# Kernel tuning notes

Measured on AMD Instinct MI355X. Metric: run time of the kernel, lower is better.

Reference implementation:

```python
import jax, jax.numpy as jnp
import numpy as np

GAMMA = 0.5
BATCH, DIM, UNITS = 16384, 512, 1024


def setup_inputs() -> dict:
    key = jax.random.key(0)
    k1, k2 = jax.random.split(key)
    inputs = jax.random.normal(k1, (BATCH, DIM), dtype=jnp.float32)
    mu = jax.random.normal(k2, (DIM, UNITS), dtype=jnp.float32)
    return {"inputs": inputs, "mu": mu}


def reference(inputs, mu):
    # Squared L2 distance from each input row to each center (column of mu):
    x_sq = jnp.sum(inputs * inputs, axis=1, keepdims=True)        # [B, 1]
    mu_sq = jnp.sum(mu * mu, axis=0, keepdims=True)               # [1, U]
    cross = inputs @ mu                                           # [B, U] GEMM
    l2 = x_sq - 2.0 * cross + mu_sq                                # [B, U]
    return jnp.exp(-GAMMA * l2)
```

## Files before the change

kernel.cpp:

```cpp
#include <hip/hip_runtime.h>
#include <hip/hip_bf16.h>

#define BATCH 16384
#define DIM   512
#define UNITS 1024

typedef float v16f __attribute__((ext_vector_type(16)));

#define APITCH 516
#define BPITCH 33

__device__ __forceinline__ void async_copy16(const void* g, void* l) {
    __builtin_amdgcn_global_load_lds(
        (const __attribute__((address_space(1))) void*)g,
        (__attribute__((address_space(3))) void*)l,
        16 , 0 , 0 );
}

__global__ __launch_bounds__(256)
void prep_kernel(const float* __restrict__ in, const float* __restrict__ mu,
                 unsigned char* __restrict__ A8f, unsigned char* __restrict__ B8f,
                 float* __restrict__ xsq, float* __restrict__ musq) {
    __shared__ __attribute__((aligned(16))) char smem[512 * BPITCH * 4 + 1024];
    const int t  = threadIdx.x;
    const int l  = t & 63, w = t >> 6;
    const int ln = l & 31, h = l >> 5;

    if (blockIdx.x >= UNITS / 32) {
        float* lds = (float*)smem;
        float* red = (float*)(smem + 32 * APITCH * 4);
        const int bb = blockIdx.x - UNITS / 32;
        const int c  = (bb & 7) * 64 + (bb >> 3);
        const float4* src = (const float4*)(in + (size_t)c * 32 * DIM);
        float4* l4 = (float4*)lds;
#pragma unroll
        for (int i = 0; i < 16; i++) {
            const int f = i * 256 + t;
            l4[(f >> 7) * (APITCH / 4) + (f & 127)] = src[f];
        }
        __syncthreads();
        float s = 0.f;
#pragma unroll
        for (int j = 0; j < 8; j++) {
            const int kw = w * 8 + j;
            const float* p = lds + ln * APITCH + kw * 16 + h * 8;
            float4 f0 = *(const float4*)p;
            float4 f1 = *(const float4*)(p + 4);
            s += f0.x * f0.x + f0.y * f0.y + f0.z * f0.z + f0.w * f0.w
               + f1.x * f1.x + f1.y * f1.y + f1.z * f1.z + f1.w * f1.w;
            int lo = __builtin_amdgcn_cvt_pk_fp8_f32(f0.x, f0.y, 0, false);
            lo     = __builtin_amdgcn_cvt_pk_fp8_f32(f0.z, f0.w, lo, true);
            int hi = __builtin_amdgcn_cvt_pk_fp8_f32(f1.x, f1.y, 0, false);
            hi     = __builtin_amdgcn_cvt_pk_fp8_f32(f1.z, f1.w, hi, true);
            *(int2*)(A8f + (((size_t)c * 32 + kw) * 64 + l) * 8) = make_int2(lo, hi);
        }
        red[ln * 8 + w * 2 + h] = s;
        __syncthreads();
        if (t < 32) {
            float a = 0.f;
#pragma unroll
            for (int i = 0; i < 8; i++) a += red[t * 8 + i];
            xsq[c * 32 + t] = a;
        }
    } else {
        float* lds = (float*)smem;
        float* red = (float*)(smem + 512 * BPITCH * 4);
        const int nb = blockIdx.x;
        const int n0 = nb * 32;
        const int col = t & 31, kg = t >> 5;
        float s = 0.f;
        for (int i = 0; i < 64; i++) {
            const int k = i * 8 + kg;
            float v = mu[(size_t)k * UNITS + n0 + col];
            s += v * v;
            lds[k * BPITCH + col] = v;
        }
        red[col * 8 + kg] = s;
        __syncthreads();
        if (t < 32) {
            float a = 0.f;
#pragma unroll
            for (int i = 0; i < 8; i++) a += red[t * 8 + i];
            musq[n0 + t] = a;
        }
#pragma unroll
        for (int j = 0; j < 8; j++) {
            const int kw = w * 8 + j;
            const float* p = lds + (kw * 16 + h * 8) * BPITCH + ln;
            float f[8];
#pragma unroll
            for (int i = 0; i < 8; i++) f[i] = p[i * BPITCH];
            int lo = __builtin_amdgcn_cvt_pk_fp8_f32(f[0], f[1], 0, false);
            lo     = __builtin_amdgcn_cvt_pk_fp8_f32(f[2], f[3], lo, true);
            int hi = __builtin_amdgcn_cvt_pk_fp8_f32(f[4], f[5], 0, false);
            hi     = __builtin_amdgcn_cvt_pk_fp8_f32(f[6], f[7], hi, true);
            *(int2*)(B8f + (((size_t)nb * 32 + kw) * 64 + l) * 8) = make_int2(lo, hi);
        }
    }
}

__global__ __launch_bounds__(1024, 4)
void rbf_gemm_kernel(const unsigned char* __restrict__ A8f,
                     const unsigned char* __restrict__ B8f,
                     const float* __restrict__ xsq,
                     const float* __restrict__ musq,
                     float* __restrict__ out) {
    __shared__ __attribute__((aligned(16))) unsigned char Bs[131072];

    const int t  = threadIdx.x;
    const int l  = t & 63;
    const int w  = t >> 6;
    const int ln = l & 31;
    const int h  = l >> 5;

    const int b  = blockIdx.x;
    const int x  = b & 7;
    const int j  = b >> 3;
    const int mt = x * 8 + (j & 7);
    const int nt = j >> 3;
    const int m0 = mt * 256;
    const int n0 = nt * 256;
    const int wm = (w >> 2) * 64;
    const int wn = (w & 3) * 64;

    const unsigned char* bsrc = B8f + (size_t)n0 * 512;
#pragma unroll
    for (int i = 0; i < 8; i++) {
        const int c = i * 1024 + t;
        async_copy16(bsrc + c * 16, Bs + c * 16);
    }
    __syncthreads();

    const long* Af  = (const long*)A8f + (size_t)((m0 + wm) >> 5) * 2048 + l;
    const long* lbp = (const long*)Bs + (size_t)(wn >> 5) * 2048 + l;

    v16f acc[2][2];
#pragma unroll
    for (int c = 0; c < 2; c++)
#pragma unroll
        for (int g = 0; g < 2; g++) acc[c][g] = (v16f)0.f;

#pragma unroll 4
    for (int kw = 0; kw < 32; kw++) {
        long a0 = Af[kw * 64];
        long a1 = Af[2048 + kw * 64];
        long b0 = lbp[kw * 64];
        long b1 = lbp[2048 + kw * 64];
        acc[0][0] = __builtin_amdgcn_mfma_f32_32x32x16_fp8_fp8(a0, b0, acc[0][0], 0, 0, 0);
        acc[0][1] = __builtin_amdgcn_mfma_f32_32x32x16_fp8_fp8(a0, b1, acc[0][1], 0, 0, 0);
        acc[1][0] = __builtin_amdgcn_mfma_f32_32x32x16_fp8_fp8(a1, b0, acc[1][0], 0, 0, 0);
        acc[1][1] = __builtin_amdgcn_mfma_f32_32x32x16_fp8_fp8(a1, b1, acc[1][1], 0, 0, 0);
    }

#pragma unroll
    for (int c = 0; c < 2; c++) {
        const int mc = m0 + wm + c * 32;
        const float xv = -0.5f * xsq[mc + ln];
#pragma unroll
        for (int g = 0; g < 2; g++) {
            const int nc = n0 + wn + g * 32;
            const float mb = -0.5f * musq[nc + ln];
#pragma unroll
            for (int r = 0; r < 16; r++) {
                const int rl = (r & 3) + 8 * (r >> 2) + 4 * h;
                const float xb = __shfl(xv, rl, 64);
                float v = __expf(acc[c][g][r] + xb + mb);
                __builtin_nontemporal_store(
                    v, out + (size_t)(mc + rl) * UNITS + nc + ln);
            }
        }
    }
}

extern "C" void kernel_launch(void* const* d_in, const int* in_sizes, int n_in,
                              void* d_out, int out_size, void* d_ws, size_t ws_size,
                              hipStream_t stream) {
    const float* inputs = (const float*)d_in[0];
    const float* mu     = (const float*)d_in[1];
    float* out = (float*)d_out;

    char* ws = (char*)d_ws;
    unsigned char* A8f = (unsigned char*)ws;
    unsigned char* B8f = (unsigned char*)(ws + (size_t)BATCH * DIM);
    float* xsq  = (float*)(ws + (size_t)BATCH * DIM + (size_t)UNITS * DIM);
    float* musq = xsq + BATCH;

    prep_kernel<<<UNITS / 32 + BATCH / 32, 256, 0, stream>>>(
        inputs, mu, A8f, B8f, xsq, musq);
    rbf_gemm_kernel<<<256, 1024, 0, stream>>>(A8f, B8f, xsq, musq, out);
}
```

Before: 111.3 us.

## Fuse fp8 conversion and norm computation into the RBF GEMM kernel

Removes the separate prep kernel and workspace. Each block converts its A rows to fp8 on the fly, double-buffered in LDS with loads prefetched one step ahead, and converts its mu column slice to fp8 in LDS while computing squared norms locally. This saves a launch and the intermediate global round trip. In exchange, mu conversion is repeated across m-tiles and A is read as fp32 by each n-tile, and the K loop now carries a barrier per step.

Result: slower. 117.4 us (+5.5%).

```diff
diff --git a/kernel.cpp b/kernel.cpp
--- a/kernel.cpp
+++ b/kernel.cpp
@@ -1,5 +1,4 @@
 #include <hip/hip_runtime.h>
-#include <hip/hip_bf16.h>
 
 #define BATCH 16384
 #define DIM   512
@@ -7,105 +6,18 @@
 
 typedef float v16f __attribute__((ext_vector_type(16)));
 
-#define APITCH 516
-#define BPITCH 33
-
-__device__ __forceinline__ void async_copy16(const void* g, void* l) {
-    __builtin_amdgcn_global_load_lds(
-        (const __attribute__((address_space(1))) void*)g,
-        (__attribute__((address_space(3))) void*)l,
-        16 , 0 , 0 );
-}
-
-__global__ __launch_bounds__(256)
-void prep_kernel(const float* __restrict__ in, const float* __restrict__ mu,
-                 unsigned char* __restrict__ A8f, unsigned char* __restrict__ B8f,
-                 float* __restrict__ xsq, float* __restrict__ musq) {
-    __shared__ __attribute__((aligned(16))) char smem[512 * BPITCH * 4 + 1024];
-    const int t  = threadIdx.x;
-    const int l  = t & 63, w = t >> 6;
-    const int ln = l & 31, h = l >> 5;
-
-    if (blockIdx.x >= UNITS / 32) {
-        float* lds = (float*)smem;
-        float* red = (float*)(smem + 32 * APITCH * 4);
-        const int bb = blockIdx.x - UNITS / 32;
-        const int c  = (bb & 7) * 64 + (bb >> 3);
-        const float4* src = (const float4*)(in + (size_t)c * 32 * DIM);
-        float4* l4 = (float4*)lds;
-#pragma unroll
-        for (int i = 0; i < 16; i++) {
-            const int f = i * 256 + t;
-            l4[(f >> 7) * (APITCH / 4) + (f & 127)] = src[f];
-        }
-        __syncthreads();
-        float s = 0.f;
-#pragma unroll
-        for (int j = 0; j < 8; j++) {
-            const int kw = w * 8 + j;
-            const float* p = lds + ln * APITCH + kw * 16 + h * 8;
-            float4 f0 = *(const float4*)p;
-            float4 f1 = *(const float4*)(p + 4);
-            s += f0.x * f0.x + f0.y * f0.y + f0.z * f0.z + f0.w * f0.w
-               + f1.x * f1.x + f1.y * f1.y + f1.z * f1.z + f1.w * f1.w;
-            int lo = __builtin_amdgcn_cvt_pk_fp8_f32(f0.x, f0.y, 0, false);
-            lo     = __builtin_amdgcn_cvt_pk_fp8_f32(f0.z, f0.w, lo, true);
-            int hi = __builtin_amdgcn_cvt_pk_fp8_f32(f1.x, f1.y, 0, false);
-            hi     = __builtin_amdgcn_cvt_pk_fp8_f32(f1.z, f1.w, hi, true);
-            *(int2*)(A8f + (((size_t)c * 32 + kw) * 64 + l) * 8) = make_int2(lo, hi);
-        }
-        red[ln * 8 + w * 2 + h] = s;
-        __syncthreads();
-        if (t < 32) {
-            float a = 0.f;
-#pragma unroll
-            for (int i = 0; i < 8; i++) a += red[t * 8 + i];
-            xsq[c * 32 + t] = a;
-        }
-    } else {
-        float* lds = (float*)smem;
-        float* red = (float*)(smem + 512 * BPITCH * 4);
-        const int nb = blockIdx.x;
-        const int n0 = nb * 32;
-        const int col = t & 31, kg = t >> 5;
-        float s = 0.f;
-        for (int i = 0; i < 64; i++) {
-            const int k = i * 8 + kg;
-            float v = mu[(size_t)k * UNITS + n0 + col];
-            s += v * v;
-            lds[k * BPITCH + col] = v;
-        }
-        red[col * 8 + kg] = s;
-        __syncthreads();
-        if (t < 32) {
-            float a = 0.f;
-#pragma unroll
-            for (int i = 0; i < 8; i++) a += red[t * 8 + i];
-            musq[n0 + t] = a;
-        }
-#pragma unroll
-        for (int j = 0; j < 8; j++) {
-            const int kw = w * 8 + j;
-            const float* p = lds + (kw * 16 + h * 8) * BPITCH + ln;
-            float f[8];
-#pragma unroll
-            for (int i = 0; i < 8; i++) f[i] = p[i * BPITCH];
-            int lo = __builtin_amdgcn_cvt_pk_fp8_f32(f[0], f[1], 0, false);
-            lo     = __builtin_amdgcn_cvt_pk_fp8_f32(f[2], f[3], lo, true);
-            int hi = __builtin_amdgcn_cvt_pk_fp8_f32(f[4], f[5], 0, false);
-            hi     = __builtin_amdgcn_cvt_pk_fp8_f32(f[6], f[7], hi, true);
-            *(int2*)(B8f + (((size_t)nb * 32 + kw) * 64 + l) * 8) = make_int2(lo, hi);
-        }
-    }
-}
+#define MFMA(a, b, c) __builtin_amdgcn_mfma_f32_32x32x16_fp8_fp8((a), (b), (c), 0, 0, 0)
 
 __global__ __launch_bounds__(1024, 4)
-void rbf_gemm_kernel(const unsigned char* __restrict__ A8f,
-                     const unsigned char* __restrict__ B8f,
-                     const float* __restrict__ xsq,
-                     const float* __restrict__ musq,
-                     float* __restrict__ out) {
-    __shared__ __attribute__((aligned(16))) unsigned char Bs[131072];
+void rbf_fused_kernel(const float* __restrict__ in, const float* __restrict__ mu,
+                      float* __restrict__ out) {
+    __shared__ __attribute__((aligned(16))) unsigned char smem[155648];
+    unsigned char* Bs = smem;
+    unsigned char* As = smem + 131072;
+    float* xsq_red  = (float*)(smem + 147456);
+    float* musq_red = (float*)(smem + 151552);
+    float* xsq_l    = (float*)(smem + 153600);
+    float* musq_l   = (float*)(smem + 154624);
 
     const int t  = threadIdx.x;
     const int l  = t & 63;
@@ -113,60 +25,122 @@
     const int ln = l & 31;
     const int h  = l >> 5;
 
-    const int b  = blockIdx.x;
-    const int x  = b & 7;
-    const int j  = b >> 3;
-    const int mt = x * 8 + (j & 7);
-    const int nt = j >> 3;
-    const int m0 = mt * 256;
-    const int n0 = nt * 256;
-    const int wm = (w >> 2) * 64;
-    const int wn = (w & 3) * 64;
+    const int b   = blockIdx.x;
+    const int xcd = b & 7;
+    const int j   = b >> 3;
+    const int m0  = (xcd * 8 + (j & 7)) * 256;
+    const int n0  = (j >> 3) * 256;
+    const int wm  = (w >> 2) * 64;
+    const int wn  = (w & 3) * 64;
 
-    const unsigned char* bsrc = B8f + (size_t)n0 * 512;
+    const int ar = t >> 2, ap = t & 3;
+    const float* arow = in + (size_t)(m0 + ar) * DIM + ap * 8;
+    const int aidx = ((((ar >> 5) * 2 + (ap >> 1)) * 64) + (ap & 1) * 32 + (ar & 31)) * 8;
+
+    float4 g0 = *(const float4*)(arow + 0);
+    float4 g1 = *(const float4*)(arow + 4);
+
+    {
+        const int ng  = w >> 1;
+        const int kwb = (w & 1) * 16;
+        const float* msrc = mu + (size_t)(kwb * 16 + h * 8) * UNITS + n0 + ng * 32 + ln;
+        unsigned char* bdst = Bs + ((ng * 32 + kwb) * 64 + l) * 8;
+        float s = 0.f;
+#pragma unroll 4
+        for (int kk = 0; kk < 16; kk++) {
+            float v[8];
 #pragma unroll
-    for (int i = 0; i < 8; i++) {
-        const int c = i * 1024 + t;
-        async_copy16(bsrc + c * 16, Bs + c * 16);
+            for (int jj = 0; jj < 8; jj++) v[jj] = msrc[(size_t)(kk * 16 + jj) * UNITS];
+#pragma unroll
+            for (int jj = 0; jj < 8; jj++) s += v[jj] * v[jj];
+            int lo = __builtin_amdgcn_cvt_pk_fp8_f32(v[0], v[1], 0, false);
+            lo     = __builtin_amdgcn_cvt_pk_fp8_f32(v[2], v[3], lo, true);
+            int hi = __builtin_amdgcn_cvt_pk_fp8_f32(v[4], v[5], 0, false);
+            hi     = __builtin_amdgcn_cvt_pk_fp8_f32(v[6], v[7], hi, true);
+            *(int2*)(bdst + kk * 512) = make_int2(lo, hi);
+        }
+        s += __shfl_xor(s, 32, 64);
+        if (h == 0) musq_red[(ng * 32 + ln) * 2 + (w & 1)] = s;
+    }
+
+    float sA = g0.x * g0.x + g0.y * g0.y + g0.z * g0.z + g0.w * g0.w
+             + g1.x * g1.x + g1.y * g1.y + g1.z * g1.z + g1.w * g1.w;
+    {
+        int lo = __builtin_amdgcn_cvt_pk_fp8_f32(g0.x, g0.y, 0, false);
+        lo     = __builtin_amdgcn_cvt_pk_fp8_f32(g0.z, g0.w, lo, true);
+        int hi = __builtin_amdgcn_cvt_pk_fp8_f32(g1.x, g1.y, 0, false);
+        hi     = __builtin_amdgcn_cvt_pk_fp8_f32(g1.z, g1.w, hi, true);
+        *(int2*)(As + aidx) = make_int2(lo, hi);
     }
     __syncthreads();
+    if (t < 256) musq_l[t] = -0.5f * (musq_red[t * 2] + musq_red[t * 2 + 1]);
 
-    const long* Af  = (const long*)A8f + (size_t)((m0 + wm) >> 5) * 2048 + l;
-    const long* lbp = (const long*)Bs + (size_t)(wn >> 5) * 2048 + l;
-
+    const long* BsL = (const long*)Bs;
     v16f acc[2][2];
 #pragma unroll
     for (int c = 0; c < 2; c++)
 #pragma unroll
         for (int g = 0; g < 2; g++) acc[c][g] = (v16f)0.f;
 
-#pragma unroll 4
-    for (int kw = 0; kw < 32; kw++) {
-        long a0 = Af[kw * 64];
-        long a1 = Af[2048 + kw * 64];
-        long b0 = lbp[kw * 64];
-        long b1 = lbp[2048 + kw * 64];
-        acc[0][0] = __builtin_amdgcn_mfma_f32_32x32x16_fp8_fp8(a0, b0, acc[0][0], 0, 0, 0);
-        acc[0][1] = __builtin_amdgcn_mfma_f32_32x32x16_fp8_fp8(a0, b1, acc[0][1], 0, 0, 0);
-        acc[1][0] = __builtin_amdgcn_mfma_f32_32x32x16_fp8_fp8(a1, b0, acc[1][0], 0, 0, 0);
-        acc[1][1] = __builtin_amdgcn_mfma_f32_32x32x16_fp8_fp8(a1, b1, acc[1][1], 0, 0, 0);
+#pragma unroll 2
+    for (int i = 0; i < 16; i++) {
+        float4 f0, f1;
+        if (i < 15) {
+            f0 = *(const float4*)(arow + (i + 1) * 32);
+            f1 = *(const float4*)(arow + (i + 1) * 32 + 4);
+        }
+        const long* AsL = (const long*)(As + (i & 1) * 8192);
+        long a[2][2], bb[2][2];
+#pragma unroll
+        for (int c = 0; c < 2; c++)
+#pragma unroll
+            for (int kh = 0; kh < 2; kh++)
+                a[c][kh] = AsL[(((w >> 2) * 2 + c) * 2 + kh) * 64 + l];
+#pragma unroll
+        for (int g = 0; g < 2; g++)
+#pragma unroll
+            for (int kh = 0; kh < 2; kh++)
+                bb[g][kh] = BsL[(((w & 3) * 2 + g) * 32 + 2 * i + kh) * 64 + l];
+#pragma unroll
+        for (int kh = 0; kh < 2; kh++) {
+            acc[0][0] = MFMA(a[0][kh], bb[0][kh], acc[0][0]);
+            acc[0][1] = MFMA(a[0][kh], bb[1][kh], acc[0][1]);
+            acc[1][0] = MFMA(a[1][kh], bb[0][kh], acc[1][0]);
+            acc[1][1] = MFMA(a[1][kh], bb[1][kh], acc[1][1]);
+        }
+        if (i < 15) {
+            sA += f0.x * f0.x + f0.y * f0.y + f0.z * f0.z + f0.w * f0.w
+                + f1.x * f1.x + f1.y * f1.y + f1.z * f1.z + f1.w * f1.w;
+            int lo = __builtin_amdgcn_cvt_pk_fp8_f32(f0.x, f0.y, 0, false);
+            lo     = __builtin_amdgcn_cvt_pk_fp8_f32(f0.z, f0.w, lo, true);
+            int hi = __builtin_amdgcn_cvt_pk_fp8_f32(f1.x, f1.y, 0, false);
+            hi     = __builtin_amdgcn_cvt_pk_fp8_f32(f1.z, f1.w, hi, true);
+            *(int2*)(As + ((i + 1) & 1) * 8192 + aidx) = make_int2(lo, hi);
+        }
+        __syncthreads();
     }
+
+    xsq_red[ar * 4 + ap] = sA;
+    __syncthreads();
+    if (t < 256)
+        xsq_l[t] = -0.5f * (xsq_red[t * 4] + xsq_red[t * 4 + 1]
+                          + xsq_red[t * 4 + 2] + xsq_red[t * 4 + 3]);
+    __syncthreads();
 
 #pragma unroll
     for (int c = 0; c < 2; c++) {
-        const int mc = m0 + wm + c * 32;
-        const float xv = -0.5f * xsq[mc + ln];
+        const size_t mrow = m0 + wm + c * 32;
 #pragma unroll
         for (int g = 0; g < 2; g++) {
             const int nc = n0 + wn + g * 32;
-            const float mb = -0.5f * musq[nc + ln];
+            const float mb = musq_l[wn + g * 32 + ln];
 #pragma unroll
             for (int r = 0; r < 16; r++) {
                 const int rl = (r & 3) + 8 * (r >> 2) + 4 * h;
-                const float xb = __shfl(xv, rl, 64);
+                const float xb = xsq_l[wm + c * 32 + rl];
                 float v = __expf(acc[c][g][r] + xb + mb);
                 __builtin_nontemporal_store(
-                    v, out + (size_t)(mc + rl) * UNITS + nc + ln);
+                    v, out + (mrow + rl) * UNITS + nc + ln);
             }
         }
     }
@@ -178,14 +152,7 @@
     const float* inputs = (const float*)d_in[0];
     const float* mu     = (const float*)d_in[1];
     float* out = (float*)d_out;
+    (void)d_ws; (void)ws_size;
 
-    char* ws = (char*)d_ws;
-    unsigned char* A8f = (unsigned char*)ws;
-    unsigned char* B8f = (unsigned char*)(ws + (size_t)BATCH * DIM);
-    float* xsq  = (float*)(ws + (size_t)BATCH * DIM + (size_t)UNITS * DIM);
-    float* musq = xsq + BATCH;
-
-    prep_kernel<<<UNITS / 32 + BATCH / 32, 256, 0, stream>>>(
-        inputs, mu, A8f, B8f, xsq, musq);
-    rbf_gemm_kernel<<<256, 1024, 0, stream>>>(A8f, B8f, xsq, musq, out);
+    rbf_fused_kernel<<<256, 1024, 0, stream>>>(inputs, mu, out);
 }
```

## Shrink GEMM block tile to 256x128 and split warp work into two passes

Applied to the files above, without the earlier changes.

Halves the per-block N tile (256x128, 512 threads, 64KB LDS) and doubles the grid to 512 blocks. Each warp now computes its two 32-row strips sequentially with two accumulators, running the epilogue after each strip, so fewer accumulators are live at once. This is meant to raise occupancy and let the exp/store epilogue of one strip overlap with other blocks' MFMA work. In exchange, A rows are fetched twice as often across blocks and each A fragment is reused across fewer MFMAs.

Result: no change. 110.9 us (-0.3%).

```diff
diff --git a/kernel.cpp b/kernel.cpp
--- a/kernel.cpp
+++ b/kernel.cpp
@@ -9,6 +9,8 @@
 
 #define APITCH 516
 #define BPITCH 33
+
+#define MFMA_F8(a, b, c) __builtin_amdgcn_mfma_f32_32x32x16_fp8_fp8((a), (b), (c), 0, 0, 0)
 
 __device__ __forceinline__ void async_copy16(const void* g, void* l) {
     __builtin_amdgcn_global_load_lds(
@@ -99,13 +101,13 @@
     }
 }
 
-__global__ __launch_bounds__(1024, 4)
+__global__ __launch_bounds__(512, 4)
 void rbf_gemm_kernel(const unsigned char* __restrict__ A8f,
                      const unsigned char* __restrict__ B8f,
                      const float* __restrict__ xsq,
                      const float* __restrict__ musq,
                      float* __restrict__ out) {
-    __shared__ __attribute__((aligned(16))) unsigned char Bs[131072];
+    __shared__ __attribute__((aligned(16))) unsigned char Bs[65536];
 
     const int t  = threadIdx.x;
     const int l  = t & 63;
@@ -113,61 +115,51 @@
     const int ln = l & 31;
     const int h  = l >> 5;
 
-    const int b  = blockIdx.x;
-    const int x  = b & 7;
-    const int j  = b >> 3;
-    const int mt = x * 8 + (j & 7);
-    const int nt = j >> 3;
-    const int m0 = mt * 256;
-    const int n0 = nt * 256;
-    const int wm = (w >> 2) * 64;
-    const int wn = (w & 3) * 64;
+    const int b   = blockIdx.x;
+    const int xcd = b & 7;
+    const int j   = b >> 3;
+    const int m0  = (xcd * 8 + (j & 7)) * 256;
+    const int n0  = (j >> 3) * 128;
+    const int wm  = (w >> 1) * 64;
+    const int wn  = (w & 1) * 64;
 
     const unsigned char* bsrc = B8f + (size_t)n0 * 512;
 #pragma unroll
     for (int i = 0; i < 8; i++) {
-        const int c = i * 1024 + t;
+        const int c = i * 512 + t;
         async_copy16(bsrc + c * 16, Bs + c * 16);
     }
     __syncthreads();
 
-    const long* Af  = (const long*)A8f + (size_t)((m0 + wm) >> 5) * 2048 + l;
-    const long* lbp = (const long*)Bs + (size_t)(wn >> 5) * 2048 + l;
-
-    v16f acc[2][2];
-#pragma unroll
-    for (int c = 0; c < 2; c++)
-#pragma unroll
-        for (int g = 0; g < 2; g++) acc[c][g] = (v16f)0.f;
-
-#pragma unroll 4
-    for (int kw = 0; kw < 32; kw++) {
-        long a0 = Af[kw * 64];
-        long a1 = Af[2048 + kw * 64];
-        long b0 = lbp[kw * 64];
-        long b1 = lbp[2048 + kw * 64];
-        acc[0][0] = __builtin_amdgcn_mfma_f32_32x32x16_fp8_fp8(a0, b0, acc[0][0], 0, 0, 0);
-        acc[0][1] = __builtin_amdgcn_mfma_f32_32x32x16_fp8_fp8(a0, b1, acc[0][1], 0, 0, 0);
-        acc[1][0] = __builtin_amdgcn_mfma_f32_32x32x16_fp8_fp8(a1, b0, acc[1][0], 0, 0, 0);
-        acc[1][1] = __builtin_amdgcn_mfma_f32_32x32x16_fp8_fp8(a1, b1, acc[1][1], 0, 0, 0);
-    }
+    const long* BsL = (const long*)Bs;
+    const long* Bp  = BsL + (size_t)(wn >> 5) * 2048 + l;
 
 #pragma unroll
-    for (int c = 0; c < 2; c++) {
-        const int mc = m0 + wm + c * 32;
-        const float xv = -0.5f * xsq[mc + ln];
+    for (int p = 0; p < 2; p++) {
+        const int mbase = m0 + wm + p * 32;
+        const long* Af = (const long*)A8f + (size_t)(mbase >> 5) * 2048 + l;
+
+        v16f acc0 = (v16f)0.f, acc1 = (v16f)0.f;
+#pragma unroll 4
+        for (int kw = 0; kw < 32; kw++) {
+            long a  = Af[kw * 64];
+            long b0 = Bp[kw * 64];
+            long b1 = Bp[2048 + kw * 64];
+            acc0 = MFMA_F8(a, b0, acc0);
+            acc1 = MFMA_F8(a, b1, acc1);
+        }
+
+        const float xv  = -0.5f * xsq[mbase + ln];
+        const float mb0 = -0.5f * musq[n0 + wn + ln];
+        const float mb1 = -0.5f * musq[n0 + wn + 32 + ln];
+        float* obase = out + n0 + wn + ln;
 #pragma unroll
-        for (int g = 0; g < 2; g++) {
-            const int nc = n0 + wn + g * 32;
-            const float mb = -0.5f * musq[nc + ln];
-#pragma unroll
-            for (int r = 0; r < 16; r++) {
-                const int rl = (r & 3) + 8 * (r >> 2) + 4 * h;
-                const float xb = __shfl(xv, rl, 64);
-                float v = __expf(acc[c][g][r] + xb + mb);
-                __builtin_nontemporal_store(
-                    v, out + (size_t)(mc + rl) * UNITS + nc + ln);
-            }
+        for (int r = 0; r < 16; r++) {
+            const int rl = (r & 3) + 8 * (r >> 2) + 4 * h;
+            const float xb = __shfl(xv, rl, 64);
+            float* orow = obase + (size_t)(mbase + rl) * UNITS;
+            __builtin_nontemporal_store(__expf(acc0[r] + xb + mb0), orow);
+            __builtin_nontemporal_store(__expf(acc1[r] + xb + mb1), orow + 32);
         }
     }
 }
@@ -187,5 +179,5 @@
 
     prep_kernel<<<UNITS / 32 + BATCH / 32, 256, 0, stream>>>(
         inputs, mu, A8f, B8f, xsq, musq);
-    rbf_gemm_kernel<<<256, 1024, 0, stream>>>(A8f, B8f, xsq, musq, out);
+    rbf_gemm_kernel<<<512, 512, 0, stream>>>(A8f, B8f, xsq, musq, out);
 }
```
